# Optimization experiments

Measured on AMD Instinct MI355X. Metric: run time of the kernel, lower is better.

## Reference

```python
import jax, jax.numpy as jnp
import numpy as np

N = 50000          # nodes
E = 800000         # edges (avg degree 16)
HID = 128          # hidden_dim
NUM_RBF = 32
CUTOFF = 6.0
LIGAND_NODE = 0
D_IN = 3 * HID + NUM_RBF + 1  # 417


def setup_inputs() -> dict:
    key = jax.random.key(0)
    ks = jax.random.split(key, 16)
    s = 0.05
    return {
        "h": jax.random.normal(ks[0], (N, HID), dtype=jnp.float32),
        "pos": jax.random.normal(ks[1], (N, 3), dtype=jnp.float32) * 3.0,
        "edge_index": jax.random.randint(ks[2], (2, E), 0, N, dtype=jnp.int32),
        "edge_type": jax.random.randint(ks[3], (E,), 0, 2, dtype=jnp.int32),
        "node_type": jax.random.randint(ks[4], (N,), 0, 2, dtype=jnp.int32),
        "emb": jax.random.normal(ks[5], (2, HID), dtype=jnp.float32) * s,
        "mw1": jax.random.normal(ks[6], (D_IN, HID), dtype=jnp.float32) * s,
        "mb1": jnp.zeros((HID,), dtype=jnp.float32),
        "mw2": jax.random.normal(ks[7], (HID, HID), dtype=jnp.float32) * s,
        "mb2": jnp.zeros((HID,), dtype=jnp.float32),
        "uw1": jax.random.normal(ks[8], (2 * HID, HID), dtype=jnp.float32) * s,
        "ub1": jnp.zeros((HID,), dtype=jnp.float32),
        "uw2": jax.random.normal(ks[9], (HID, HID), dtype=jnp.float32) * s,
        "ub2": jnp.zeros((HID,), dtype=jnp.float32),
        "ln_g": jnp.ones((HID,), dtype=jnp.float32),
        "ln_b": jnp.zeros((HID,), dtype=jnp.float32),
    }


def _silu(x):
    return x * jax.nn.sigmoid(x)


def _layernorm(x, g, b, eps=1e-5):
    mu = jnp.mean(x, axis=-1, keepdims=True)
    var = jnp.var(x, axis=-1, keepdims=True)
    return (x - mu) * jax.lax.rsqrt(var + eps) * g + b


def reference(h, pos, edge_index, edge_type, node_type,
              emb, mw1, mb1, mw2, mb2, uw1, ub1, uw2, ub2, ln_g, ln_b):
    # Gaussian RBF setup (matches torch.linspace(0, cutoff, num_rbf))
    centers = jnp.linspace(0.0, CUTOFF, NUM_RBF)          # [R]
    step = CUTOFF / (NUM_RBF - 1)
    gamma = 1.0 / max(step * step, 1e-6)

    src, dst = edge_index[0], edge_index[1]               # [E]
    rel = pos[src] - pos[dst]                             # [E,3]
    dist = jnp.linalg.norm(rel, axis=-1)                  # [E]
    radial = jnp.exp(-gamma * (dist[:, None] - centers[None, :]) ** 2)  # [E,R]
    edge_kind = emb[edge_type]                            # [E,H]

    # edge message MLP (dropout in eval mode = identity)
    m_in = jnp.concatenate([h[src], h[dst], edge_kind, radial, dist[:, None]], axis=-1)  # [E, 3H+R+1]
    x = _silu(m_in @ mw1 + mb1)
    messages = _silu(x @ mw2 + mb2)                       # [E,H]

    # scatter-mean over dst into N nodes
    sums = jax.ops.segment_sum(messages, dst, num_segments=N)           # [N,H]
    counts = jax.ops.segment_sum(jnp.ones((E,), dtype=h.dtype), dst, num_segments=N)
    aggregated = sums / jnp.maximum(counts, 1.0)[:, None]

    # node update MLP
    u = _silu(jnp.concatenate([h, aggregated], axis=-1) @ uw1 + ub1)
    update = u @ uw2 + ub2                                # [N,H]

    # masked residual + LayerNorm (only ligand nodes updated)
    normed = _layernorm(h + update, ln_g, ln_b)
    ligand_mask = (node_type == LIGAND_NODE)[:, None]
    return jnp.where(ligand_mask, normed, h)
```

## Files before the change

### kernel.cpp

```cpp
#include <hip/hip_runtime.h>
#include <hip/hip_bf16.h>
#include <math.h>

#define NN   50000
#define NE   800000
#define HID  128
#define NRBF 32
#define NSCAN_BLOCKS ((NN + 255) / 256)

typedef __attribute__((ext_vector_type(8))) short short8;
typedef __attribute__((ext_vector_type(4))) float floatx4;

constexpr int TILE_N = 64;

__device__ __forceinline__ float silu_f(float x) {
  return x / (1.0f + __expf(-x));
}
__device__ __forceinline__ ushort f2bf(float f) {
  __hip_bfloat16 b = __float2bfloat16(f);
  return *reinterpret_cast<ushort*>(&b);
}
__device__ __forceinline__ float bf2f(ushort u) {
  union { uint u32; float f; } c; c.u32 = ((uint)u) << 16; return c.f;
}

__global__ void counts_i_kernel(const int* __restrict__ edge_index, int* __restrict__ cnt) {
  const int e = blockIdx.x * blockDim.x + threadIdx.x;
  if (e < NE) atomicAdd(&cnt[edge_index[NE + e]], 1);
}

__global__ void scan_a_kernel(const int* __restrict__ cnt, int* __restrict__ incl,
                              int* __restrict__ bsum) {
  __shared__ int s[256];
  const int i = blockIdx.x * 256 + threadIdx.x;
  const int v = (i < NN) ? cnt[i] : 0;
  s[threadIdx.x] = v;
  __syncthreads();
  for (int off = 1; off < 256; off <<= 1) {
    const int x = (threadIdx.x >= off) ? s[threadIdx.x - off] : 0;
    __syncthreads();
    s[threadIdx.x] += x;
    __syncthreads();
  }
  if (i < NN) incl[i] = s[threadIdx.x];
  if (threadIdx.x == 255) bsum[blockIdx.x] = s[255];
}

__global__ void scan_b_kernel(int* __restrict__ bsum, int nb) {
  __shared__ int s[256];
  const int v = (threadIdx.x < nb) ? bsum[threadIdx.x] : 0;
  s[threadIdx.x] = v;
  __syncthreads();
  for (int off = 1; off < 256; off <<= 1) {
    const int x = (threadIdx.x >= off) ? s[threadIdx.x - off] : 0;
    __syncthreads();
    s[threadIdx.x] += x;
    __syncthreads();
  }
  bsum[threadIdx.x] = s[threadIdx.x] - v;
}

__global__ void scan_c_kernel(int* __restrict__ incl, const int* __restrict__ cnt,
                              const int* __restrict__ bsumex, float* __restrict__ cf) {
  const int i = blockIdx.x * 256 + threadIdx.x;
  if (i < NN) {
    const int c = cnt[i];
    incl[i] = incl[i] - c + bsumex[blockIdx.x];
    cf[i] = (float)c;
  }
}

__global__ void perm_kernel(const int* __restrict__ edge_index, const int* __restrict__ edge_type,
                            const int* __restrict__ starts,
                            int* __restrict__ cursor, int2* __restrict__ rec) {
  const int e = blockIdx.x * blockDim.x + threadIdx.x;
  if (e < NE) {
    const int s  = edge_index[e];
    const int d  = edge_index[NE + e];
    const int et = edge_type[e];
    const int pos = atomicAdd(&cursor[d], 1);
    rec[starts[d] + pos] = make_int2(s | (et << 24), d);
  }
}

__global__ void embp_kernel(const float* __restrict__ emb, const float* __restrict__ mw1,
                            const float* __restrict__ mb1, float* __restrict__ embp) {
  const int t = threadIdx.x;
  const int row = t >> 7, col = t & 127;
  float s = mb1[col];
  #pragma unroll 4
  for (int k = 0; k < HID; ++k)
    s = fmaf(emb[row * HID + k], mw1[(256 + k) * HID + col], s);
  embp[row * HID + col] = s;
}

__global__ void build_w1x_kernel(const float* __restrict__ mw1, const float* __restrict__ embp,
                                 float* __restrict__ w1x) {
  const int tid = blockIdx.x * 256 + threadIdx.x;
  if (tid >= 64 * 128) return;
  const int r = tid >> 7, c = tid & 127;
  float v = 0.0f;
  if (r < 32)       v = mw1[(384 + r) * HID + c];
  else if (r == 32) v = mw1[416 * HID + c];
  else if (r == 33) v = embp[c];
  else if (r == 34) v = embp[HID + c];
  w1x[tid] = v;
}

__global__ void pack_w_kernel(const float* __restrict__ W, ushort* __restrict__ out,
                              int Korig, int nks) {
  const int tid = blockIdx.x * blockDim.x + threadIdx.x;
  if (tid >= nks * 8 * 64) return;
  const int l = tid & 63;
  const int c = (tid >> 6) & 7;
  const int kk = tid >> 9;
  union { ushort u[8]; uint4 v; } o;
  #pragma unroll
  for (int j = 0; j < 8; ++j) {
    const int k = kk * 32 + ((l >> 4) * 8) + j;
    const float f = (k < Korig) ? W[k * HID + c * 16 + (l & 15)] : 0.0f;
    o.u[j] = f2bf(f);
  }
  reinterpret_cast<uint4*>(out)[tid] = o.v;
}

__global__ __launch_bounds__(256, 3)
void proj_kernel(const float* __restrict__ h,
                 const ushort* __restrict__ wap, const ushort* __restrict__ wbp,
                 ushort* __restrict__ hs_proj, ushort* __restrict__ hd_proj)
{
  __shared__ __align__(16) ushort sH[64 * HID];
  char* const sHb = reinterpret_cast<char*>(sH);
  const int t  = threadIdx.x;
  const int n0 = blockIdx.x * 64;

  {
    const int e = t >> 2, c0 = (t & 3) * 32;
    const int node = n0 + e;
    const int sm = (e & 7) << 4;
    #pragma unroll
    for (int m = 0; m < 4; ++m) {
      const int c = c0 + m * 8;
      float4 f0 = make_float4(0,0,0,0), f1 = f0;
      if (node < NN) {
        f0 = *reinterpret_cast<const float4*>(h + (long)node * HID + c);
        f1 = *reinterpret_cast<const float4*>(h + (long)node * HID + c + 4);
      }
      union { ushort u[8]; uint4 v; } o;
      o.u[0]=f2bf(f0.x); o.u[1]=f2bf(f0.y); o.u[2]=f2bf(f0.z); o.u[3]=f2bf(f0.w);
      o.u[4]=f2bf(f1.x); o.u[5]=f2bf(f1.y); o.u[6]=f2bf(f1.z); o.u[7]=f2bf(f1.w);
      *reinterpret_cast<uint4*>(sHb + ((e * 256 + c * 2) ^ sm)) = o.v;
    }
  }
  __syncthreads();

  const int lane = t & 63;
  const int w    = t >> 6;
  const int rt0  = (w & 1) * 2;
  const int ct0  = (w >> 1) * 4;
  const int lrow = lane & 15;
  const int lk16 = (lane >> 4) * 16;
  const int rowA0 = rt0 * 16 + lrow, rowA1 = rowA0 + 16;
  const int smA0 = (rowA0 & 7) << 4, smA1 = (rowA1 & 7) << 4;

  floatx4 accA[2][4] = {}, accB[2][4] = {};
  const ushort* const baseA = wap + ((size_t)ct0 * 64 + lane) * 8;
  const ushort* const baseB = wbp + ((size_t)ct0 * 64 + lane) * 8;
  #pragma unroll
  for (int kk = 0; kk < 4; ++kk) {
    short8 afr[2];
    afr[0] = *reinterpret_cast<const short8*>(sHb + rowA0 * 256 + ((kk*64 + lk16) ^ smA0));
    afr[1] = *reinterpret_cast<const short8*>(sHb + rowA1 * 256 + ((kk*64 + lk16) ^ smA1));
    #pragma unroll
    for (int j = 0; j < 4; ++j) {
      const short8 bA = *reinterpret_cast<const short8*>(baseA + kk * 4096 + j * 512);
      const short8 bB = *reinterpret_cast<const short8*>(baseB + kk * 4096 + j * 512);
      #pragma unroll
      for (int i = 0; i < 2; ++i) {
        accA[i][j] = __builtin_amdgcn_mfma_f32_16x16x32_bf16(afr[i], bA, accA[i][j], 0, 0, 0);
        accB[i][j] = __builtin_amdgcn_mfma_f32_16x16x32_bf16(afr[i], bB, accB[i][j], 0, 0, 0);
      }
    }
  }
  #pragma unroll
  for (int i = 0; i < 2; ++i)
    #pragma unroll
    for (int r = 0; r < 4; ++r) {
      const int row = (rt0 + i) * 16 + (lane >> 4) * 4 + r;
      const int node = n0 + row;
      if (node < NN) {
        #pragma unroll
        for (int j = 0; j < 4; ++j) {
          const int col = (ct0 + j) * 16 + lrow;
          hs_proj[(long)node * HID + col] = f2bf(accA[i][j][r]);
          hd_proj[(long)node * HID + col] = f2bf(accB[i][j][r]);
        }
      }
    }
}

__global__ __launch_bounds__(256, 4)
void edge_kernel(const ushort* __restrict__ hs_proj, const ushort* __restrict__ hd_proj,
                 const float* __restrict__ pos, const int2* __restrict__ rec,
                 const ushort* __restrict__ w1xp, const ushort* __restrict__ w2p,
                 const float* __restrict__ mb2,
                 float* sums)
{
  __shared__ __align__(16) char sBuf[20480];
  __shared__ int   sDst[64];
  __shared__ int   sEt[64];
  __shared__ float sDistF[64];

  const int t  = threadIdx.x;
  const int e0 = blockIdx.x * 64;
  const int e  = t >> 2, q = t & 3;

  const int2 rc = rec[e0 + e];
  const int src = rc.x & 0x00FFFFFF;
  const int et  = ((unsigned)rc.x) >> 24;
  const int dst = rc.y;

  const float dx = pos[3*src]   - pos[3*dst];
  const float dy = pos[3*src+1] - pos[3*dst+1];
  const float dz = pos[3*src+2] - pos[3*dst+2];
  const float dist = sqrtf(dx*dx + dy*dy + dz*dz);
  if (q == 0) { sDst[e] = dst; sEt[e] = et; sDistF[e] = dist; }

  {
    const ushort* const hsr = hs_proj + (long)src * HID;
    const ushort* const hdr = hd_proj + (long)dst * HID;
    const int sm = (e & 7) << 4;
    #pragma unroll
    for (int m = 0; m < 4; ++m) {
      const int c = q * 32 + m * 8;
      const uint4 a = *reinterpret_cast<const uint4*>(hsr + c);
      const uint4 b = *reinterpret_cast<const uint4*>(hdr + c);
      const ushort* au = reinterpret_cast<const ushort*>(&a);
      const ushort* bu = reinterpret_cast<const ushort*>(&b);
      union { ushort u[8]; uint4 v; } o;
      #pragma unroll
      for (int j = 0; j < 8; ++j) o.u[j] = f2bf(bf2f(au[j]) + bf2f(bu[j]));
      *reinterpret_cast<uint4*>(sBuf + ((e * 256 + c * 2) ^ sm)) = o.v;
    }
    const float step  = 6.0f / 31.0f;
    const float gamma = 1.0f / (step * step);
    const int r0 = q * 8;
    union { ushort u[8]; uint4 v; } o;
    #pragma unroll
    for (int j = 0; j < 8; ++j) {
      const float dd = dist - step * (float)(r0 + j);
      o.u[j] = f2bf(__expf(-gamma * dd * dd));
    }
    reinterpret_cast<uint4*>(sBuf + 16384)[e * 4 + (q ^ (e & 3))] = o.v;
  }
  __syncthreads();

  const int lane = t & 63;
  const int w    = t >> 6;
  const int rt0  = (w & 1) * 2;
  const int ct0  = (w >> 1) * 4;
  const int lrow = lane & 15;
  const int lk16 = (lane >> 4) * 16;
  const int rowA0 = rt0 * 16 + lrow, rowA1 = rowA0 + 16;
  const int smA0 = (rowA0 & 7) << 4, smA1 = (rowA1 & 7) << 4;

  floatx4 acc[2][4];
  #pragma unroll
  for (int i = 0; i < 2; ++i)
    #pragma unroll
    for (int r = 0; r < 4; ++r) {
      const int row = (rt0 + i) * 16 + (lane >> 4) * 4 + r;
      const int sm = (row & 7) << 4;
      #pragma unroll
      for (int j = 0; j < 4; ++j) {
        const int col = (ct0 + j) * 16 + lrow;
        acc[i][j][r] = bf2f(*reinterpret_cast<const ushort*>(
            sBuf + row * 256 + ((col * 2) ^ sm)));
      }
    }
  {
    const uint4* const sRbf = reinterpret_cast<const uint4*>(sBuf + 16384);
    const short8 a0 = *reinterpret_cast<const short8*>(&sRbf[rowA0 * 4 + ((lane >> 4) ^ (rowA0 & 3))]);
    const short8 a1 = *reinterpret_cast<const short8*>(&sRbf[rowA1 * 4 + ((lane >> 4) ^ (rowA1 & 3))]);
    const ushort* const bb = w1xp + ((size_t)ct0 * 64 + lane) * 8;
    #pragma unroll
    for (int j = 0; j < 4; ++j) {
      const short8 b = *reinterpret_cast<const short8*>(bb + j * 512);
      acc[0][j] = __builtin_amdgcn_mfma_f32_16x16x32_bf16(a0, b, acc[0][j], 0, 0, 0);
      acc[1][j] = __builtin_amdgcn_mfma_f32_16x16x32_bf16(a1, b, acc[1][j], 0, 0, 0);
    }
    short8 x0 = {0,0,0,0,0,0,0,0}, x1 = {0,0,0,0,0,0,0,0};
    if ((lane >> 4) == 0) {
      x0[0] = (short)f2bf(sDistF[rowA0]);
      x0[1] = (sEt[rowA0] == 0) ? (short)0x3F80 : (short)0;
      x0[2] = (sEt[rowA0] == 1) ? (short)0x3F80 : (short)0;
      x1[0] = (short)f2bf(sDistF[rowA1]);
      x1[1] = (sEt[rowA1] == 0) ? (short)0x3F80 : (short)0;
      x1[2] = (sEt[rowA1] == 1) ? (short)0x3F80 : (short)0;
    }
    #pragma unroll
    for (int j = 0; j < 4; ++j) {
      const short8 b = *reinterpret_cast<const short8*>(bb + 4096 + j * 512);
      acc[0][j] = __builtin_amdgcn_mfma_f32_16x16x32_bf16(x0, b, acc[0][j], 0, 0, 0);
      acc[1][j] = __builtin_amdgcn_mfma_f32_16x16x32_bf16(x1, b, acc[1][j], 0, 0, 0);
    }
  }

  #pragma unroll
  for (int i = 0; i < 2; ++i)
    #pragma unroll
    for (int r = 0; r < 4; ++r) {
      const int row = (rt0 + i) * 16 + (lane >> 4) * 4 + r;
      const int sm = (row & 7) << 4;
      #pragma unroll
      for (int j = 0; j < 4; ++j) {
        const int col = (ct0 + j) * 16 + lrow;
        *reinterpret_cast<ushort*>(sBuf + row * 256 + ((col * 2) ^ sm)) =
            f2bf(silu_f(acc[i][j][r]));
      }
    }
  __syncthreads();

  floatx4 acc2[2][4] = {};
  {
    const ushort* const bbase = w2p + ((size_t)ct0 * 64 + lane) * 8;
    #pragma unroll 2
    for (int kk = 0; kk < 4; ++kk) {
      short8 bfr[4];
      #pragma unroll
      for (int j = 0; j < 4; ++j)
        bfr[j] = *reinterpret_cast<const short8*>(bbase + kk * 4096 + j * 512);
      short8 afr[2];
      afr[0] = *reinterpret_cast<const short8*>(sBuf + rowA0 * 256 + ((kk*64 + lk16) ^ smA0));
      afr[1] = *reinterpret_cast<const short8*>(sBuf + rowA1 * 256 + ((kk*64 + lk16) ^ smA1));
      #pragma unroll
      for (int i = 0; i < 2; ++i)
        #pragma unroll
        for (int j = 0; j < 4; ++j)
          acc2[i][j] = __builtin_amdgcn_mfma_f32_16x16x32_bf16(afr[i], bfr[j], acc2[i][j], 0, 0, 0);
    }
  }
  __syncthreads();

  {
    float b2v[4];
    #pragma unroll
    for (int j = 0; j < 4; ++j) b2v[j] = mb2[(ct0 + j) * 16 + lrow];
    #pragma unroll
    for (int i = 0; i < 2; ++i)
      #pragma unroll
      for (int r = 0; r < 4; ++r) {
        const int row = (rt0 + i) * 16 + (lane >> 4) * 4 + r;
        const int sm = (row & 7) << 4;
        #pragma unroll
        for (int j = 0; j < 4; ++j) {
          const int col = (ct0 + j) * 16 + lrow;
          *reinterpret_cast<ushort*>(sBuf + row * 256 + ((col * 2) ^ sm)) =
              f2bf(silu_f(acc2[i][j][r] + b2v[j]));
        }
      }
  }
  __syncthreads();

  {
    const int half = t >> 7;
    const int c    = t & 127;
    const int r0   = half * 32;
    int cur = sDst[r0];
    float accv = 0.0f;
    for (int r = r0; r < r0 + 32; ++r) {
      const int d = sDst[r];
      const float mv = bf2f(*reinterpret_cast<const ushort*>(
          sBuf + r * 256 + ((c * 2) ^ ((r & 7) << 4))));
      if (d != cur) {
        atomicAdd(&sums[(long)cur * HID + c], accv);
        accv = 0.0f;
        cur = d;
      }
      accv += mv;
    }
    atomicAdd(&sums[(long)cur * HID + c], accv);
  }
}

__global__ __launch_bounds__(256, 4)
void node_kernel(const float* __restrict__ h,
                 const float* sums, const float* __restrict__ counts,
                 const int* __restrict__ node_type,
                 const float* __restrict__ uw1, const float* __restrict__ ub1,
                 const float* __restrict__ uw2, const float* __restrict__ ub2,
                 const float* __restrict__ ln_g, const float* __restrict__ ln_b,
                 float* out)
{
  __shared__ ushort sIn[TILE_N * 256];

  const int t  = threadIdx.x;
  const int n0 = blockIdx.x * TILE_N;

  for (int idx = t; idx < TILE_N*HID; idx += 256) {
    const int n = idx >> 7, c = idx & (HID-1);
    const int node = n0 + n;
    float hv = 0.f, av = 0.f;
    if (node < NN) {
      hv = h[(long)node*HID + c];
      av = sums[(long)node*HID + c] / fmaxf(counts[node], 1.0f);
    }
    sIn[n*256 + c]       = f2bf(hv);
    sIn[n*256 + HID + c] = f2bf(av);
  }
  __syncthreads();

  const int tx = t & 31;
  const int ty = t >> 5;

  const float* wp = uw1 + tx*4;
  float4 acc[8];
  #pragma unroll
  for (int i = 0; i < 8; ++i) acc[i] = make_float4(0.f,0.f,0.f,0.f);
  for (int k = 0; k < 2*HID; ++k) {
    const float4 w = *reinterpret_cast<const float4*>(wp + (long)k*HID);
    #pragma unroll
    for (int i = 0; i < 8; ++i) {
      const float a = bf2f(sIn[(ty*8+i)*256 + k]);
      acc[i].x = fmaf(a, w.x, acc[i].x);
      acc[i].y = fmaf(a, w.y, acc[i].y);
      acc[i].z = fmaf(a, w.z, acc[i].z);
      acc[i].w = fmaf(a, w.w, acc[i].w);
    }
  }
  __syncthreads();

  const float4 b1 = *reinterpret_cast<const float4*>(ub1 + tx*4);
  #pragma unroll
  for (int i = 0; i < 8; ++i) {
    const int e = ty*8 + i;
    float4 v = acc[i];
    ushort4 s;
    s.x = f2bf(silu_f(v.x + b1.x)); s.y = f2bf(silu_f(v.y + b1.y));
    s.z = f2bf(silu_f(v.z + b1.z)); s.w = f2bf(silu_f(v.w + b1.w));
    *reinterpret_cast<ushort4*>(&sIn[e*256 + tx*4]) = s;
  }
  __syncthreads();

  const float* wp2 = uw2 + tx*4;
  float4 acc2[8];
  #pragma unroll
  for (int i = 0; i < 8; ++i) acc2[i] = make_float4(0.f,0.f,0.f,0.f);
  for (int k = 0; k < HID; ++k) {
    const float4 w = *reinterpret_cast<const float4*>(wp2 + (long)k*HID);
    #pragma unroll
    for (int i = 0; i < 8; ++i) {
      const float a = bf2f(sIn[(ty*8+i)*256 + k]);
      acc2[i].x = fmaf(a, w.x, acc2[i].x);
      acc2[i].y = fmaf(a, w.y, acc2[i].y);
      acc2[i].z = fmaf(a, w.z, acc2[i].z);
      acc2[i].w = fmaf(a, w.w, acc2[i].w);
    }
  }
  const float4 b2 = *reinterpret_cast<const float4*>(ub2 + tx*4);
  #pragma unroll
  for (int i = 0; i < 8; ++i) {
    const int e = ty*8 + i;
    ushort4 s;
    s.x = f2bf(acc2[i].x + b2.x); s.y = f2bf(acc2[i].y + b2.y);
    s.z = f2bf(acc2[i].z + b2.z); s.w = f2bf(acc2[i].w + b2.w);
    *reinterpret_cast<ushort4*>(&sIn[e*256 + HID + tx*4]) = s;
  }
  __syncthreads();

  {
    const int n = t >> 2, q = t & 3;
    const int node = n0 + n;
    if (node < NN) {
      float4 hv4[8], xv4[8];
      float smm = 0.f, sqq = 0.f;
      #pragma unroll
      for (int m = 0; m < 8; ++m) {
        const int c = q * 32 + m * 4;
        const ushort4 us = *reinterpret_cast<const ushort4*>(&sIn[n*256 + HID + c]);
        const float4 hv = *reinterpret_cast<const float4*>(h + (long)node * HID + c);
        float4 x;
        x.x = hv.x + bf2f(us.x); x.y = hv.y + bf2f(us.y);
        x.z = hv.z + bf2f(us.z); x.w = hv.w + bf2f(us.w);
        hv4[m] = hv; xv4[m] = x;
        smm += x.x + x.y + x.z + x.w;
        sqq += x.x*x.x + x.y*x.y + x.z*x.z + x.w*x.w;
      }
      smm += __shfl_xor(smm, 1); sqq += __shfl_xor(sqq, 1);
      smm += __shfl_xor(smm, 2); sqq += __shfl_xor(sqq, 2);
      const float mu = smm * (1.0f / HID);
      float var = sqq * (1.0f / HID) - mu * mu;
      var = fmaxf(var, 0.0f);
      const float rs = rsqrtf(var + 1e-5f);
      const bool lig = (node_type[node] == 0);
      #pragma unroll
      for (int m = 0; m < 8; ++m) {
        const int c = q * 32 + m * 4;
        const float4 g = *reinterpret_cast<const float4*>(ln_g + c);
        const float4 b = *reinterpret_cast<const float4*>(ln_b + c);
        float4 o;
        o.x = lig ? (xv4[m].x - mu) * rs * g.x + b.x : hv4[m].x;
        o.y = lig ? (xv4[m].y - mu) * rs * g.y + b.y : hv4[m].y;
        o.z = lig ? (xv4[m].z - mu) * rs * g.z + b.z : hv4[m].z;
        o.w = lig ? (xv4[m].w - mu) * rs * g.w + b.w : hv4[m].w;
        *reinterpret_cast<float4*>(out + (long)node * HID + c) = o;
      }
    }
  }
}

extern "C" void kernel_launch(void* const* d_in, const int* in_sizes, int n_in,
                              void* d_out, int out_size, void* d_ws, size_t ws_size,
                              hipStream_t stream)
{
  const float* h    = (const float*)d_in[0];
  const float* pos  = (const float*)d_in[1];
  const int*   eidx = (const int*)  d_in[2];
  const int*   etyp = (const int*)  d_in[3];
  const int*   ntyp = (const int*)  d_in[4];
  const float* emb  = (const float*)d_in[5];
  const float* mw1  = (const float*)d_in[6];
  const float* mb1  = (const float*)d_in[7];
  const float* mw2  = (const float*)d_in[8];
  const float* mb2  = (const float*)d_in[9];
  const float* uw1  = (const float*)d_in[10];
  const float* ub1  = (const float*)d_in[11];
  const float* uw2  = (const float*)d_in[12];
  const float* ub2  = (const float*)d_in[13];
  const float* lng  = (const float*)d_in[14];
  const float* lnb  = (const float*)d_in[15];

  float* sums = (float*)d_out;

  float*  counts_f = (float*)d_ws;
  ushort* hs_proj  = (ushort*)(counts_f + NN);
  ushort* hd_proj  = hs_proj + (long)NN*HID;
  float*  embp     = (float*)(hd_proj + (long)NN*HID);
  float*  w1x      = embp + 256;
  ushort* wap      = (ushort*)(w1x + 64*128);
  ushort* wbp      = wap  + 4*4096;
  ushort* w1xp     = wbp  + 4*4096;
  ushort* w2p      = w1xp + 2*4096;
  int*    cnt_i    = (int*)(w2p + 4*4096);
  int*    cursor   = cnt_i + NN;
  int*    starts   = cursor + NN;
  int*    bsum     = starts + NN;
  int2*   rec      = (int2*)(bsum + 256);

  hipMemsetAsync(sums, 0, (size_t)NN*HID*4, stream);
  hipMemsetAsync(cnt_i, 0, (size_t)NN*2*4, stream);

  counts_i_kernel<<<(NE + 255)/256, 256, 0, stream>>>(eidx, cnt_i);
  scan_a_kernel<<<NSCAN_BLOCKS, 256, 0, stream>>>(cnt_i, starts, bsum);
  scan_b_kernel<<<1, 256, 0, stream>>>(bsum, NSCAN_BLOCKS);
  scan_c_kernel<<<NSCAN_BLOCKS, 256, 0, stream>>>(starts, cnt_i, bsum, counts_f);
  perm_kernel<<<(NE + 255)/256, 256, 0, stream>>>(eidx, etyp, starts, cursor, rec);

  embp_kernel<<<1, 256, 0, stream>>>(emb, mw1, mb1, embp);
  build_w1x_kernel<<<32, 256, 0, stream>>>(mw1, embp, w1x);
  pack_w_kernel<<<8, 256, 0, stream>>>(mw1,           wap,  128, 4);
  pack_w_kernel<<<8, 256, 0, stream>>>(mw1 + 128*HID, wbp,  128, 4);
  pack_w_kernel<<<4, 256, 0, stream>>>(w1x,           w1xp,  64, 2);
  pack_w_kernel<<<8, 256, 0, stream>>>(mw2,           w2p,  128, 4);

  proj_kernel<<<(NN + 63)/64, 256, 0, stream>>>(h, wap, wbp, hs_proj, hd_proj);
  edge_kernel<<<NE/64, 256, 0, stream>>>(hs_proj, hd_proj, pos, rec,
                                         w1xp, w2p, mb2, sums);
  node_kernel<<<(NN + 63)/64, 256, 0, stream>>>(h, sums, counts_f, ntyp,
                                                uw1, ub1, uw2, ub2,
                                                lng, lnb, (float*)d_out);
}
```

Measured before the change: 420.3 us.

## Fuse node projections into edge kernel, gathering raw bf16 features

```diff
diff --git a/kernel.cpp b/kernel.cpp
--- a/kernel.cpp
+++ b/kernel.cpp
@@ -81,6 +81,17 @@
     const int pos = atomicAdd(&cursor[d], 1);
     rec[starts[d] + pos] = make_int2(s | (et << 24), d);
   }
+}
+
+__global__ void convert_h_kernel(const float* __restrict__ h, ushort* __restrict__ hb) {
+  const int tid = blockIdx.x * blockDim.x + threadIdx.x;
+  if (tid >= NN * HID / 8) return;
+  const float4 f0 = reinterpret_cast<const float4*>(h)[tid * 2];
+  const float4 f1 = reinterpret_cast<const float4*>(h)[tid * 2 + 1];
+  union { ushort u[8]; uint4 v; } o;
+  o.u[0] = f2bf(f0.x); o.u[1] = f2bf(f0.y); o.u[2] = f2bf(f0.z); o.u[3] = f2bf(f0.w);
+  o.u[4] = f2bf(f1.x); o.u[5] = f2bf(f1.y); o.u[6] = f2bf(f1.z); o.u[7] = f2bf(f1.w);
+  reinterpret_cast<uint4*>(hb)[tid] = o.v;
 }
 
 __global__ void embp_kernel(const float* __restrict__ emb, const float* __restrict__ mw1,
@@ -124,33 +135,55 @@
   reinterpret_cast<uint4*>(out)[tid] = o.v;
 }
 
-__global__ __launch_bounds__(256, 3)
-void proj_kernel(const float* __restrict__ h,
+__global__ __launch_bounds__(256, 4)
+void edge_kernel(const ushort* __restrict__ hb,
+                 const float* __restrict__ pos, const int2* __restrict__ rec,
                  const ushort* __restrict__ wap, const ushort* __restrict__ wbp,
-                 ushort* __restrict__ hs_proj, ushort* __restrict__ hd_proj)
+                 const ushort* __restrict__ w1xp, const ushort* __restrict__ w2p,
+                 const float* __restrict__ mb2,
+                 float* sums)
 {
-  __shared__ __align__(16) ushort sH[64 * HID];
-  char* const sHb = reinterpret_cast<char*>(sH);
+  __shared__ __align__(16) char  sBuf[16384];
+  __shared__ __align__(16) uint4 sRbf[256];
+  __shared__ int   sDst[64];
+  __shared__ int   sEt[64];
+  __shared__ float sDistF[64];
+
   const int t  = threadIdx.x;
-  const int n0 = blockIdx.x * 64;
-
-  {
-    const int e = t >> 2, c0 = (t & 3) * 32;
-    const int node = n0 + e;
-    const int sm = (e & 7) << 4;
+  const int e0 = blockIdx.x * 64;
+  const int e  = t >> 2, q = t & 3;
+
+  const int2 rc = rec[e0 + e];
+  const int src = rc.x & 0x00FFFFFF;
+  const int et  = ((unsigned)rc.x) >> 24;
+  const int dst = rc.y;
+
+  const float dx = pos[3*src]   - pos[3*dst];
+  const float dy = pos[3*src+1] - pos[3*dst+1];
+  const float dz = pos[3*src+2] - pos[3*dst+2];
+  const float dist = sqrtf(dx*dx + dy*dy + dz*dz);
+  if (q == 0) { sDst[e] = dst; sEt[e] = et; sDistF[e] = dist; }
+
+  const int sm = (e & 7) << 4;
+
+  {
+    const ushort* const hr = hb + (long)src * HID;
     #pragma unroll
     for (int m = 0; m < 4; ++m) {
-      const int c = c0 + m * 8;
-      float4 f0 = make_float4(0,0,0,0), f1 = f0;
-      if (node < NN) {
-        f0 = *reinterpret_cast<const float4*>(h + (long)node * HID + c);
-        f1 = *reinterpret_cast<const float4*>(h + (long)node * HID + c + 4);
-      }
-      union { ushort u[8]; uint4 v; } o;
-      o.u[0]=f2bf(f0.x); o.u[1]=f2bf(f0.y); o.u[2]=f2bf(f0.z); o.u[3]=f2bf(f0.w);
-      o.u[4]=f2bf(f1.x); o.u[5]=f2bf(f1.y); o.u[6]=f2bf(f1.z); o.u[7]=f2bf(f1.w);
-      *reinterpret_cast<uint4*>(sHb + ((e * 256 + c * 2) ^ sm)) = o.v;
-    }
+      const int c = q * 32 + m * 8;
+      const uint4 v = *reinterpret_cast<const uint4*>(hr + c);
+      *reinterpret_cast<uint4*>(sBuf + ((e * 256 + c * 2) ^ sm)) = v;
+    }
+    const float step  = 6.0f / 31.0f;
+    const float gamma = 1.0f / (step * step);
+    const int r0 = q * 8;
+    union { ushort u[8]; uint4 v; } o;
+    #pragma unroll
+    for (int j = 0; j < 8; ++j) {
+      const float dd = dist - step * (float)(r0 + j);
+      o.u[j] = f2bf(__expf(-gamma * dd * dd));
+    }
+    sRbf[e * 4 + (q ^ (e & 3))] = o.v;
   }
   __syncthreads();
 
@@ -163,123 +196,52 @@
   const int rowA0 = rt0 * 16 + lrow, rowA1 = rowA0 + 16;
   const int smA0 = (rowA0 & 7) << 4, smA1 = (rowA1 & 7) << 4;
 
-  floatx4 accA[2][4] = {}, accB[2][4] = {};
-  const ushort* const baseA = wap + ((size_t)ct0 * 64 + lane) * 8;
-  const ushort* const baseB = wbp + ((size_t)ct0 * 64 + lane) * 8;
-  #pragma unroll
-  for (int kk = 0; kk < 4; ++kk) {
-    short8 afr[2];
-    afr[0] = *reinterpret_cast<const short8*>(sHb + rowA0 * 256 + ((kk*64 + lk16) ^ smA0));
-    afr[1] = *reinterpret_cast<const short8*>(sHb + rowA1 * 256 + ((kk*64 + lk16) ^ smA1));
-    #pragma unroll
-    for (int j = 0; j < 4; ++j) {
-      const short8 bA = *reinterpret_cast<const short8*>(baseA + kk * 4096 + j * 512);
-      const short8 bB = *reinterpret_cast<const short8*>(baseB + kk * 4096 + j * 512);
-      #pragma unroll
-      for (int i = 0; i < 2; ++i) {
-        accA[i][j] = __builtin_amdgcn_mfma_f32_16x16x32_bf16(afr[i], bA, accA[i][j], 0, 0, 0);
-        accB[i][j] = __builtin_amdgcn_mfma_f32_16x16x32_bf16(afr[i], bB, accB[i][j], 0, 0, 0);
-      }
-    }
-  }
-  #pragma unroll
-  for (int i = 0; i < 2; ++i)
-    #pragma unroll
-    for (int r = 0; r < 4; ++r) {
-      const int row = (rt0 + i) * 16 + (lane >> 4) * 4 + r;
-      const int node = n0 + row;
-      if (node < NN) {
-        #pragma unroll
-        for (int j = 0; j < 4; ++j) {
-          const int col = (ct0 + j) * 16 + lrow;
-          hs_proj[(long)node * HID + col] = f2bf(accA[i][j][r]);
-          hd_proj[(long)node * HID + col] = f2bf(accB[i][j][r]);
-        }
-      }
-    }
-}
-
-__global__ __launch_bounds__(256, 4)
-void edge_kernel(const ushort* __restrict__ hs_proj, const ushort* __restrict__ hd_proj,
-                 const float* __restrict__ pos, const int2* __restrict__ rec,
-                 const ushort* __restrict__ w1xp, const ushort* __restrict__ w2p,
-                 const float* __restrict__ mb2,
-                 float* sums)
-{
-  __shared__ __align__(16) char sBuf[20480];
-  __shared__ int   sDst[64];
-  __shared__ int   sEt[64];
-  __shared__ float sDistF[64];
-
-  const int t  = threadIdx.x;
-  const int e0 = blockIdx.x * 64;
-  const int e  = t >> 2, q = t & 3;
-
-  const int2 rc = rec[e0 + e];
-  const int src = rc.x & 0x00FFFFFF;
-  const int et  = ((unsigned)rc.x) >> 24;
-  const int dst = rc.y;
-
-  const float dx = pos[3*src]   - pos[3*dst];
-  const float dy = pos[3*src+1] - pos[3*dst+1];
-  const float dz = pos[3*src+2] - pos[3*dst+2];
-  const float dist = sqrtf(dx*dx + dy*dy + dz*dz);
-  if (q == 0) { sDst[e] = dst; sEt[e] = et; sDistF[e] = dist; }
-
-  {
-    const ushort* const hsr = hs_proj + (long)src * HID;
-    const ushort* const hdr = hd_proj + (long)dst * HID;
-    const int sm = (e & 7) << 4;
+  floatx4 acc[2][4] = {};
+
+  {
+    const ushort* const bbase = wap + ((size_t)ct0 * 64 + lane) * 8;
+    #pragma unroll
+    for (int kk = 0; kk < 4; ++kk) {
+      short8 afr[2];
+      afr[0] = *reinterpret_cast<const short8*>(sBuf + rowA0 * 256 + ((kk*64 + lk16) ^ smA0));
+      afr[1] = *reinterpret_cast<const short8*>(sBuf + rowA1 * 256 + ((kk*64 + lk16) ^ smA1));
+      #pragma unroll
+      for (int j = 0; j < 4; ++j) {
+        const short8 b = *reinterpret_cast<const short8*>(bbase + kk * 4096 + j * 512);
+        acc[0][j] = __builtin_amdgcn_mfma_f32_16x16x32_bf16(afr[0], b, acc[0][j], 0, 0, 0);
+        acc[1][j] = __builtin_amdgcn_mfma_f32_16x16x32_bf16(afr[1], b, acc[1][j], 0, 0, 0);
+      }
+    }
+  }
+  __syncthreads();
+
+  {
+    const ushort* const hr = hb + (long)dst * HID;
     #pragma unroll
     for (int m = 0; m < 4; ++m) {
       const int c = q * 32 + m * 8;
-      const uint4 a = *reinterpret_cast<const uint4*>(hsr + c);
-      const uint4 b = *reinterpret_cast<const uint4*>(hdr + c);
-      const ushort* au = reinterpret_cast<const ushort*>(&a);
-      const ushort* bu = reinterpret_cast<const ushort*>(&b);
-      union { ushort u[8]; uint4 v; } o;
-      #pragma unroll
-      for (int j = 0; j < 8; ++j) o.u[j] = f2bf(bf2f(au[j]) + bf2f(bu[j]));
-      *reinterpret_cast<uint4*>(sBuf + ((e * 256 + c * 2) ^ sm)) = o.v;
-    }
-    const float step  = 6.0f / 31.0f;
-    const float gamma = 1.0f / (step * step);
-    const int r0 = q * 8;
-    union { ushort u[8]; uint4 v; } o;
-    #pragma unroll
-    for (int j = 0; j < 8; ++j) {
-      const float dd = dist - step * (float)(r0 + j);
-      o.u[j] = f2bf(__expf(-gamma * dd * dd));
-    }
-    reinterpret_cast<uint4*>(sBuf + 16384)[e * 4 + (q ^ (e & 3))] = o.v;
-  }
-  __syncthreads();
-
-  const int lane = t & 63;
-  const int w    = t >> 6;
-  const int rt0  = (w & 1) * 2;
-  const int ct0  = (w >> 1) * 4;
-  const int lrow = lane & 15;
-  const int lk16 = (lane >> 4) * 16;
-  const int rowA0 = rt0 * 16 + lrow, rowA1 = rowA0 + 16;
-  const int smA0 = (rowA0 & 7) << 4, smA1 = (rowA1 & 7) << 4;
-
-  floatx4 acc[2][4];
-  #pragma unroll
-  for (int i = 0; i < 2; ++i)
-    #pragma unroll
-    for (int r = 0; r < 4; ++r) {
-      const int row = (rt0 + i) * 16 + (lane >> 4) * 4 + r;
-      const int sm = (row & 7) << 4;
+      const uint4 v = *reinterpret_cast<const uint4*>(hr + c);
+      *reinterpret_cast<uint4*>(sBuf + ((e * 256 + c * 2) ^ sm)) = v;
+    }
+  }
+  __syncthreads();
+
+  {
+    const ushort* const bbase = wbp + ((size_t)ct0 * 64 + lane) * 8;
+    #pragma unroll
+    for (int kk = 0; kk < 4; ++kk) {
+      short8 afr[2];
+      afr[0] = *reinterpret_cast<const short8*>(sBuf + rowA0 * 256 + ((kk*64 + lk16) ^ smA0));
+      afr[1] = *reinterpret_cast<const short8*>(sBuf + rowA1 * 256 + ((kk*64 + lk16) ^ smA1));
       #pragma unroll
       for (int j = 0; j < 4; ++j) {
-        const int col = (ct0 + j) * 16 + lrow;
-        acc[i][j][r] = bf2f(*reinterpret_cast<const ushort*>(
-            sBuf + row * 256 + ((col * 2) ^ sm)));
-      }
-    }
-  {
-    const uint4* const sRbf = reinterpret_cast<const uint4*>(sBuf + 16384);
+        const short8 b = *reinterpret_cast<const short8*>(bbase + kk * 4096 + j * 512);
+        acc[0][j] = __builtin_amdgcn_mfma_f32_16x16x32_bf16(afr[0], b, acc[0][j], 0, 0, 0);
+        acc[1][j] = __builtin_amdgcn_mfma_f32_16x16x32_bf16(afr[1], b, acc[1][j], 0, 0, 0);
+      }
+    }
+  }
+  {
     const short8 a0 = *reinterpret_cast<const short8*>(&sRbf[rowA0 * 4 + ((lane >> 4) ^ (rowA0 & 3))]);
     const short8 a1 = *reinterpret_cast<const short8*>(&sRbf[rowA1 * 4 + ((lane >> 4) ^ (rowA1 & 3))]);
     const ushort* const bb = w1xp + ((size_t)ct0 * 64 + lane) * 8;
@@ -305,17 +267,18 @@
       acc[1][j] = __builtin_amdgcn_mfma_f32_16x16x32_bf16(x1, b, acc[1][j], 0, 0, 0);
     }
   }
+  __syncthreads();
 
   #pragma unroll
   for (int i = 0; i < 2; ++i)
     #pragma unroll
     for (int r = 0; r < 4; ++r) {
       const int row = (rt0 + i) * 16 + (lane >> 4) * 4 + r;
-      const int sm = (row & 7) << 4;
+      const int smr = (row & 7) << 4;
       #pragma unroll
       for (int j = 0; j < 4; ++j) {
         const int col = (ct0 + j) * 16 + lrow;
-        *reinterpret_cast<ushort*>(sBuf + row * 256 + ((col * 2) ^ sm)) =
+        *reinterpret_cast<ushort*>(sBuf + row * 256 + ((col * 2) ^ smr)) =
             f2bf(silu_f(acc[i][j][r]));
       }
     }
@@ -351,11 +314,11 @@
       #pragma unroll
       for (int r = 0; r < 4; ++r) {
         const int row = (rt0 + i) * 16 + (lane >> 4) * 4 + r;
-        const int sm = (row & 7) << 4;
+        const int smr = (row & 7) << 4;
         #pragma unroll
         for (int j = 0; j < 4; ++j) {
           const int col = (ct0 + j) * 16 + lrow;
-          *reinterpret_cast<ushort*>(sBuf + row * 256 + ((col * 2) ^ sm)) =
+          *reinterpret_cast<ushort*>(sBuf + row * 256 + ((col * 2) ^ smr)) =
               f2bf(silu_f(acc2[i][j][r] + b2v[j]));
         }
       }
@@ -533,9 +496,8 @@
   float* sums = (float*)d_out;
 
   float*  counts_f = (float*)d_ws;
-  ushort* hs_proj  = (ushort*)(counts_f + NN);
-  ushort* hd_proj  = hs_proj + (long)NN*HID;
-  float*  embp     = (float*)(hd_proj + (long)NN*HID);
+  ushort* hb       = (ushort*)(counts_f + NN);
+  float*  embp     = (float*)(hb + (long)NN*HID);
   float*  w1x      = embp + 256;
   ushort* wap      = (ushort*)(w1x + 64*128);
   ushort* wbp      = wap  + 4*4096;
@@ -556,6 +518,7 @@
   scan_c_kernel<<<NSCAN_BLOCKS, 256, 0, stream>>>(starts, cnt_i, bsum, counts_f);
   perm_kernel<<<(NE + 255)/256, 256, 0, stream>>>(eidx, etyp, starts, cursor, rec);
 
+  convert_h_kernel<<<(NN*HID/8 + 255)/256, 256, 0, stream>>>(h, hb);
   embp_kernel<<<1, 256, 0, stream>>>(emb, mw1, mb1, embp);
   build_w1x_kernel<<<32, 256, 0, stream>>>(mw1, embp, w1x);
   pack_w_kernel<<<8, 256, 0, stream>>>(mw1,           wap,  128, 4);
@@ -563,8 +526,7 @@
   pack_w_kernel<<<4, 256, 0, stream>>>(w1x,           w1xp,  64, 2);
   pack_w_kernel<<<8, 256, 0, stream>>>(mw2,           w2p,  128, 4);
 
-  proj_kernel<<<(NN + 63)/64, 256, 0, stream>>>(h, wap, wbp, hs_proj, hd_proj);
-  edge_kernel<<<NE/64, 256, 0, stream>>>(hs_proj, hd_proj, pos, rec,
+  edge_kernel<<<NE/64, 256, 0, stream>>>(hb, pos, rec, wap, wbp,
                                          w1xp, w2p, mb2, sums);
   node_kernel<<<(NN + 63)/64, 256, 0, stream>>>(h, sums, counts_f, ntyp,
                                                 uw1, ub1, uw2, ub2,
```

Result: slower. 429.9 us (+2.3%).
